# Kernel tuning notes

Hardware: AMD Instinct MI355X
Metric: run time of the kernel (lower is better)

Reference implementation:

```python
import jax, jax.numpy as jnp
import numpy as np

EPS = 1e-4  # CustomLayerNorm eps used by MaskedNorm


def setup_inputs() -> dict:
    key = jax.random.key(0)
    k1, k2, k3 = jax.random.split(key, 3)
    B, T, C = 8, 4096, 1024
    y = jax.random.normal(k1, (B, T, C), dtype=jnp.float32)
    mask = jax.random.randint(k2, (B, 1, T), 0, 2, dtype=jnp.int32)
    gamma = jax.random.uniform(k3, (C,), dtype=jnp.float32)
    beta = jnp.zeros((C,), dtype=jnp.float32)
    return {"y": y, "mask": mask, "gamma": gamma, "beta": beta}


def reference(y, mask, gamma, beta):
    # y: [B, T, C]; mask: [B, 1, T] (>0 means valid token)
    B, T, C = y.shape
    m = (mask.reshape(B, T) > 0)                      # [B, T] per-token mask
    mf = m.astype(y.dtype)[..., None]                 # [B, T, 1]
    n = jnp.sum(mf)                                   # number of selected tokens
    # Per-channel stats over selected tokens (torch .mean(0)/.std(0), ddof=1)
    mean = jnp.sum(y * mf, axis=(0, 1)) / n           # [C]
    diff = (y - mean) * mf                            # zero at masked-out rows
    var = jnp.sum(diff * diff, axis=(0, 1)) / (n - 1.0)
    std = jnp.sqrt(var)                               # [C]
    normed = gamma * ((y - mean) / (std + EPS)) + beta
    # masked_scatter: normalized values at valid rows, original y elsewhere
    return jnp.where(m[..., None], normed, y)
```

## Files before the change

### kernel.cpp

```cpp
#include <hip/hip_runtime.h>
#include <math.h>

#define MN_EPS 1e-4f
#define MN_MAXRPB 64

typedef float f4v __attribute__((ext_vector_type(4)));

__device__ inline void f4add(float4& a, const float4& b) {
    a.x += b.x; a.y += b.y; a.z += b.z; a.w += b.w;
}

__device__ inline f4v mn_fma4(const f4v A, const f4v v, const f4v B) {
    f4v o;
    o.x = fmaf(A.x, v.x, B.x);
    o.y = fmaf(A.y, v.y, B.y);
    o.z = fmaf(A.z, v.z, B.z);
    o.w = fmaf(A.w, v.w, B.w);
    return o;
}

__global__ void __launch_bounds__(256) mn_stats(
    const float4* __restrict__ y4, const int* __restrict__ mask,
    float4* __restrict__ pSum, float4* __restrict__ pSq,
    float* __restrict__ pCnt, int rowsPerBlock, int C4)
{
    __shared__ int sFlag[MN_MAXRPB];
    __shared__ int sIdx[MN_MAXRPB];
    __shared__ int sNum;
    const int tid = threadIdx.x;
    const int b = blockIdx.x;
    const long r0 = (long)b * rowsPerBlock;

    for (int t = tid; t < rowsPerBlock; t += 256)
        sFlag[t] = (mask[r0 + t] > 0) ? 1 : 0;
    __syncthreads();
    if (tid == 0) {
        int n = 0;
        for (int i = 0; i < rowsPerBlock; ++i)
            if (sFlag[i]) sIdx[n++] = i;
        sNum = n;
    }
    __syncthreads();
    const int nv = sNum;

    float4 s = make_float4(0.f, 0.f, 0.f, 0.f);
    float4 q = make_float4(0.f, 0.f, 0.f, 0.f);
    #pragma unroll 4
    for (int j = 0; j < nv; ++j) {
        const float4 v = y4[(r0 + sIdx[j]) * C4 + tid];
        s.x += v.x; s.y += v.y; s.z += v.z; s.w += v.w;
        q.x = fmaf(v.x, v.x, q.x);
        q.y = fmaf(v.y, v.y, q.y);
        q.z = fmaf(v.z, v.z, q.z);
        q.w = fmaf(v.w, v.w, q.w);
    }
    pSum[(long)b * C4 + tid] = s;
    pSq [(long)b * C4 + tid] = q;
    if (tid == 0) pCnt[b] = (float)nv;
}

__global__ void __launch_bounds__(256) mn_finalize(
    const float4* __restrict__ pSum4, const float4* __restrict__ pSq4,
    const float* __restrict__ pCnt,
    const float4* __restrict__ gamma4, const float4* __restrict__ beta4,
    float4* __restrict__ aArr4, float4* __restrict__ bArr4, int P, int C4)
{
    __shared__ float4 sS[256];
    __shared__ float4 sQ[256];
    __shared__ float  sN[256];
    const int tid = threadIdx.x;
    const int c4 = blockIdx.x;

    float4 s = make_float4(0.f, 0.f, 0.f, 0.f);
    float4 q = make_float4(0.f, 0.f, 0.f, 0.f);
    float  n = 0.f;
    for (int p = tid; p < P; p += 256) {
        f4add(s, pSum4[(size_t)p * C4 + c4]);
        f4add(q, pSq4 [(size_t)p * C4 + c4]);
        n += pCnt[p];
    }
    sS[tid] = s; sQ[tid] = q; sN[tid] = n;
    __syncthreads();
    for (int off = 128; off > 0; off >>= 1) {
        if (tid < off) {
            f4add(sS[tid], sS[tid + off]);
            f4add(sQ[tid], sQ[tid + off]);
            sN[tid] += sN[tid + off];
        }
        __syncthreads();
    }
    if (tid == 0) {
        const float nn = sN[0];
        const float4 S = sS[0];
        const float4 Q = sQ[0];
        const float4 G = gamma4[c4];
        const float4 Bt = beta4[c4];
        float4 A, Bo;
        {
            const float mean = S.x / nn;
            const float var = fmaxf((Q.x - S.x * S.x / nn) / (nn - 1.0f), 0.0f);
            A.x = G.x / (sqrtf(var) + MN_EPS);
            Bo.x = Bt.x - mean * A.x;
        }
        {
            const float mean = S.y / nn;
            const float var = fmaxf((Q.y - S.y * S.y / nn) / (nn - 1.0f), 0.0f);
            A.y = G.y / (sqrtf(var) + MN_EPS);
            Bo.y = Bt.y - mean * A.y;
        }
        {
            const float mean = S.z / nn;
            const float var = fmaxf((Q.z - S.z * S.z / nn) / (nn - 1.0f), 0.0f);
            A.z = G.z / (sqrtf(var) + MN_EPS);
            Bo.z = Bt.z - mean * A.z;
        }
        {
            const float mean = S.w / nn;
            const float var = fmaxf((Q.w - S.w * S.w / nn) / (nn - 1.0f), 0.0f);
            A.w = G.w / (sqrtf(var) + MN_EPS);
            Bo.w = Bt.w - mean * A.w;
        }
        aArr4[c4] = A;
        bArr4[c4] = Bo;
    }
}

__global__ void __launch_bounds__(256) mn_apply(
    const f4v* __restrict__ y4, const int* __restrict__ mask,
    const f4v* __restrict__ aArr4, const f4v* __restrict__ bArr4,
    f4v* __restrict__ out4, int R, int C4)
{
    const int tid = threadIdx.x;
    const f4v A = aArr4[tid];
    const f4v Bv = bArr4[tid];
    const int Rmain = R & ~3;
    const int stride = gridDim.x * 4;
    for (int r = blockIdx.x * 4; r < Rmain; r += stride) {
        const long i0 = (long)r * C4 + tid;
        const int m0 = mask[r];
        const int m1 = mask[r + 1];
        const int m2 = mask[r + 2];
        const int m3 = mask[r + 3];
        f4v v0 = __builtin_nontemporal_load(y4 + i0);
        f4v v1 = __builtin_nontemporal_load(y4 + i0 + C4);
        f4v v2 = __builtin_nontemporal_load(y4 + i0 + 2 * (long)C4);
        f4v v3 = __builtin_nontemporal_load(y4 + i0 + 3 * (long)C4);
        f4v o0 = (m0 > 0) ? mn_fma4(A, v0, Bv) : v0;
        f4v o1 = (m1 > 0) ? mn_fma4(A, v1, Bv) : v1;
        f4v o2 = (m2 > 0) ? mn_fma4(A, v2, Bv) : v2;
        f4v o3 = (m3 > 0) ? mn_fma4(A, v3, Bv) : v3;
        __builtin_nontemporal_store(o0, out4 + i0);
        __builtin_nontemporal_store(o1, out4 + i0 + C4);
        __builtin_nontemporal_store(o2, out4 + i0 + 2 * (long)C4);
        __builtin_nontemporal_store(o3, out4 + i0 + 3 * (long)C4);
    }
    const int rt = Rmain + blockIdx.x;
    if (rt < R) {
        const long i0 = (long)rt * C4 + tid;
        f4v v0 = __builtin_nontemporal_load(y4 + i0);
        f4v o0 = (mask[rt] > 0) ? mn_fma4(A, v0, Bv) : v0;
        __builtin_nontemporal_store(o0, out4 + i0);
    }
}

extern "C" void kernel_launch(void* const* d_in, const int* in_sizes, int n_in,
                              void* d_out, int out_size, void* d_ws, size_t ws_size,
                              hipStream_t stream)
{
    const float* y     = (const float*)d_in[0];
    const int*   mask  = (const int*)  d_in[1];
    const float* gamma = (const float*)d_in[2];
    const float* beta  = (const float*)d_in[3];
    float* out = (float*)d_out;

    const int R  = in_sizes[1];
    const int C  = in_sizes[2];
    const int C4 = C / 4;

    int P = 512;
    while (P > 1) {
        const size_t need = ((size_t)2 * P * C + P + 2 * C) * sizeof(float);
        if (need <= ws_size && (R % P) == 0 && (R / P) <= MN_MAXRPB) break;
        P >>= 1;
    }
    const int rowsPerBlock = R / P;

    float* w    = (float*)d_ws;
    float* pSum = w;
    float* pSq  = pSum + (size_t)P * C;
    float* pCnt = pSq  + (size_t)P * C;
    float* aArr = pCnt + P;
    float* bArr = aArr + C;

    mn_stats<<<P, C4, 0, stream>>>((const float4*)y, mask,
                                   (float4*)pSum, (float4*)pSq, pCnt,
                                   rowsPerBlock, C4);

    mn_finalize<<<C4, 256, 0, stream>>>((const float4*)pSum, (const float4*)pSq,
                                        pCnt, (const float4*)gamma,
                                        (const float4*)beta,
                                        (float4*)aArr, (float4*)bArr, P, C4);

    mn_apply<<<2048, C4, 0, stream>>>((const f4v*)y, mask,
                                      (const f4v*)aArr, (const f4v*)bArr,
                                      (f4v*)out, R, C4);
}
```

Measured before the change: 253.4 us.

## Split stats rows across two thread halves with ballot-based mask compaction

The stats kernel now runs 512 threads per block, with each half of the block accumulating a separate half of the block's rows and the two halves combined through shared memory. The serial single-thread compaction of valid row indices is replaced by a wavefront ballot plus popcount prefix, one wave per half. The partial-block count drops from 512 to 256, which halves the partials the finalize kernel has to read. In exchange, each block does an extra shared-memory reduction, and fewer blocks are launched, which could hurt occupancy on a GPU with many CUs.

```diff
diff --git a/kernel.cpp b/kernel.cpp
--- a/kernel.cpp
+++ b/kernel.cpp
@@ -2,7 +2,7 @@
 #include <math.h>
 
 #define MN_EPS 1e-4f
-#define MN_MAXRPB 64
+#define MN_MAXRPB 128
 
 typedef float f4v __attribute__((ext_vector_type(4)));
 
@@ -19,44 +19,59 @@
     return o;
 }
 
-__global__ void __launch_bounds__(256) mn_stats(
+__global__ void __launch_bounds__(512) mn_stats(
     const float4* __restrict__ y4, const int* __restrict__ mask,
     float4* __restrict__ pSum, float4* __restrict__ pSq,
     float* __restrict__ pCnt, int rowsPerBlock, int C4)
 {
-    __shared__ int sFlag[MN_MAXRPB];
-    __shared__ int sIdx[MN_MAXRPB];
-    __shared__ int sNum;
+    __shared__ int sIdx[2][64];
+    __shared__ int sNum[2];
+    __shared__ float4 sS[256];
+    __shared__ float4 sQ[256];
     const int tid = threadIdx.x;
+    const int half = tid / C4;
+    const int ch = tid - half * C4;
     const int b = blockIdx.x;
     const long r0 = (long)b * rowsPerBlock;
-
-    for (int t = tid; t < rowsPerBlock; t += 256)
-        sFlag[t] = (mask[r0 + t] > 0) ? 1 : 0;
+    const int halfRows = (rowsPerBlock + 1) >> 1;
+
+    if (tid < 64 || (tid >= C4 && tid < C4 + 64)) {
+        const int h = (tid < 64) ? 0 : 1;
+        const int lane = tid & 63;
+        const int r = h * halfRows + lane;
+        const bool f = (lane < halfRows) && (r < rowsPerBlock)
+                       && (mask[r0 + r] > 0);
+        const unsigned long long bal = __ballot(f);
+        if (f) sIdx[h][(int)__popcll(bal & ((1ull << lane) - 1ull))] = r;
+        if (lane == 0) sNum[h] = (int)__popcll(bal);
+    }
     __syncthreads();
-    if (tid == 0) {
-        int n = 0;
-        for (int i = 0; i < rowsPerBlock; ++i)
-            if (sFlag[i]) sIdx[n++] = i;
-        sNum = n;
-    }
-    __syncthreads();
-    const int nv = sNum;
+    const int nv = sNum[half];
 
     float4 s = make_float4(0.f, 0.f, 0.f, 0.f);
     float4 q = make_float4(0.f, 0.f, 0.f, 0.f);
     #pragma unroll 4
     for (int j = 0; j < nv; ++j) {
-        const float4 v = y4[(r0 + sIdx[j]) * C4 + tid];
+        const float4 v = y4[(r0 + sIdx[half][j]) * C4 + ch];
         s.x += v.x; s.y += v.y; s.z += v.z; s.w += v.w;
         q.x = fmaf(v.x, v.x, q.x);
         q.y = fmaf(v.y, v.y, q.y);
         q.z = fmaf(v.z, v.z, q.z);
         q.w = fmaf(v.w, v.w, q.w);
     }
-    pSum[(long)b * C4 + tid] = s;
-    pSq [(long)b * C4 + tid] = q;
-    if (tid == 0) pCnt[b] = (float)nv;
+
+    if (half == 1) {
+        sS[ch] = make_float4(s.x, s.y, s.z, s.w);
+        sQ[ch] = make_float4(q.x, q.y, q.z, q.w);
+    }
+    __syncthreads();
+    if (half == 0) {
+        f4add(s, sS[ch]);
+        f4add(q, sQ[ch]);
+        pSum[(long)b * C4 + ch] = s;
+        pSq [(long)b * C4 + ch] = q;
+        if (ch == 0) pCnt[b] = (float)(sNum[0] + sNum[1]);
+    }
 }
 
 __global__ void __launch_bounds__(256) mn_finalize(
@@ -177,7 +192,7 @@
     const int C  = in_sizes[2];
     const int C4 = C / 4;
 
-    int P = 512;
+    int P = 256;
     while (P > 1) {
         const size_t need = ((size_t)2 * P * C + P + 2 * C) * sizeof(float);
         if (need <= ws_size && (R % P) == 0 && (R / P) <= MN_MAXRPB) break;
@@ -192,9 +207,9 @@
     float* aArr = pCnt + P;
     float* bArr = aArr + C;
 
-    mn_stats<<<P, C4, 0, stream>>>((const float4*)y, mask,
-                                   (float4*)pSum, (float4*)pSq, pCnt,
-                                   rowsPerBlock, C4);
+    mn_stats<<<P, 2 * C4, 0, stream>>>((const float4*)y, mask,
+                                       (float4*)pSum, (float4*)pSq, pCnt,
+                                       rowsPerBlock, C4);
 
     mn_finalize<<<C4, 256, 0, stream>>>((const float4*)pSum, (const float4*)pSq,
                                         pCnt, (const float4*)gamma,
```

Result: faster. 247.6 us (-2.3%).
